# Kernel optimization log

Measured on AMD Instinct MI355X. Metric: run time of the kernel, lower is better.

The kernel has to match this reference:

```python
import jax, jax.numpy as jnp
import numpy as np

B, C, L, E = 5888, 128, 16, 10   # nodes, channels, sum(2l+1), num elements
P3, P2, P1 = 23, 4, 1            # num coupling paths per correlation order


def _sparse_u(key, shape, density=0.05):
    # U matrices are Clebsch-Gordan-derived and highly sparse
    k1, k2 = jax.random.split(key)
    vals = jax.random.normal(k1, shape, dtype=jnp.float32)
    mask = (jax.random.uniform(k2, shape) < density).astype(jnp.float32)
    return vals * mask


def setup_inputs() -> dict:
    key = jax.random.key(0)
    ks = jax.random.split(key, 8)
    x = jax.random.normal(ks[0], (B, C, L), dtype=jnp.float32)      # node features
    y = jax.random.uniform(ks[1], (B, E), dtype=jnp.float32)        # element one-hot (relaxed)
    U3 = _sparse_u(ks[2], (L, L, L, P3))
    U2 = _sparse_u(ks[3], (L, L, P2))
    U1 = _sparse_u(ks[4], (L, P1))
    w3 = jax.random.normal(ks[5], (E, P3, C), dtype=jnp.float32) / P3
    w2 = jax.random.normal(ks[6], (E, P2, C), dtype=jnp.float32) / P2
    w1 = jax.random.normal(ks[7], (E, P1, C), dtype=jnp.float32) / P1
    return {"x": x, "y": y, "U3": U3, "U2": U2, "U1": U1,
            "w3": w3, "w2": w2, "w1": w1}


def reference(x, y, U3, U2, U1, w3, w2, w1):
    # --- main contraction (nu = correlation = 3, irrep_out lmax=0) ---
    # 'wxik,ekc,bci,be->bcwx'
    out = jnp.einsum('wxik,ekc,bci,be->bcwx', U3, w3, x, y, optimize=True)  # [B,C,L,L]
    # --- nu = 2: weighting then feature contraction ---
    c = jnp.einsum('wxk,ekc,be->bcwx', U2, w2, y, optimize=True) + out      # [B,C,L,L]
    out = jnp.einsum('bcwi,bci->bcw', c, x)                                  # [B,C,L]
    # --- nu = 1 ---
    c = jnp.einsum('wk,ekc,be->bcw', U1, w1, y, optimize=True) + out        # [B,C,L]
    out = jnp.einsum('bci,bci->bc', c, x)                                    # [B,C]
    return out.reshape(out.shape[0], -1)
```

## Files before the change

kernel.cpp:

```cpp
#include <hip/hip_runtime.h>
#include <utility>

using u16 = unsigned short;
using u32 = unsigned int;

typedef float  f32x4   __attribute__((ext_vector_type(4)));
typedef float  f32x16  __attribute__((ext_vector_type(16)));
typedef __bf16 bf16x8  __attribute__((ext_vector_type(8)));

#define DI __device__ __forceinline__

struct RepT { unsigned char a, b, c, t; };
struct Tables8 {
  RepT rep[488];
  RepT slotmono[976];
  int n3, n2, n1;
};

constexpr int csort3key(int w, int x, int i) {
  int a = w, b = x, c = i, t = 0;
  if (a > b) { t = a; a = b; b = t; }
  if (b > c) { t = b; b = c; c = t; }
  if (a > b) { t = a; a = b; b = t; }
  return (a << 8) | (b << 4) | c;
}
constexpr int csort2key(int a, int b) { return a <= b ? ((a << 4) | b) : ((b << 4) | a); }

constexpr Tables8 build_tables8() {
  Tables8 T = {};
  bool used3[4096] = {};
  bool used2[256] = {};
  int nr = 0;
  for (int a = 0; a < 16; a++) for (int b = a; b < 16; b++) for (int c = b; c < 16; c++) {
    const int key  = (a << 8) | (b << 4) | c;
    const int rkey = csort3key((a + 8) & 15, (b + 8) & 15, (c + 8) & 15);
    if (rkey < key) continue;
    for (int q = 0; q < 2; q++) {
      const int kk = q ? rkey : key;
      if (!used3[kk]) {
        used3[kk] = true;
        const int f = (nr >> 3) * 16 + q * 8 + (nr & 7);
        T.slotmono[f].a = (unsigned char)(kk >> 8);
        T.slotmono[f].b = (unsigned char)((kk >> 4) & 15);
        T.slotmono[f].c = (unsigned char)(kk & 15);
        T.slotmono[f].t = 3;
      }
    }
    T.rep[nr].a = (unsigned char)a; T.rep[nr].b = (unsigned char)b;
    T.rep[nr].c = (unsigned char)c; T.rep[nr].t = 3; nr++;
  }
  T.n3 = nr;
  for (int a = 0; a < 16; a++) for (int b = a; b < 16; b++) {
    const int key  = (a << 4) | b;
    const int rkey = csort2key((a + 8) & 15, (b + 8) & 15);
    if (rkey < key) continue;
    for (int q = 0; q < 2; q++) {
      const int kk = q ? rkey : key;
      if (!used2[kk]) {
        used2[kk] = true;
        const int f = (nr >> 3) * 16 + q * 8 + (nr & 7);
        T.slotmono[f].a = (unsigned char)(kk >> 4);
        T.slotmono[f].b = (unsigned char)(kk & 15);
        T.slotmono[f].c = 0;
        T.slotmono[f].t = 2;
      }
    }
    T.rep[nr].a = (unsigned char)a; T.rep[nr].b = (unsigned char)b;
    T.rep[nr].c = 0; T.rep[nr].t = 2; nr++;
  }
  T.n2 = nr;
  for (int a = 0; a < 8; a++) {
    for (int q = 0; q < 2; q++) {
      const int f = (nr >> 3) * 16 + q * 8 + (nr & 7);
      T.slotmono[f].a = (unsigned char)((a + 8 * q) & 15);
      T.slotmono[f].b = 0; T.slotmono[f].c = 0; T.slotmono[f].t = 1;
    }
    T.rep[nr].a = (unsigned char)a; T.rep[nr].b = 0; T.rep[nr].c = 0;
    T.rep[nr].t = 1; nr++;
  }
  T.n1 = nr;
  return T;
}

constexpr Tables8 TT8 = build_tables8();
static_assert(TT8.n3 == 408, "cubic rep count");
static_assert(TT8.n2 == 480, "quad rep count");
static_assert(TT8.n1 == 488, "linear rep count");

__device__ const Tables8 g_T8 = build_tables8();

#define BN 5888
#define CN 128
#define EN 10
#define NCHUNK 61

DI u16 f2bf(float f) { union { __bf16 h; u16 s; } u; u.h = (__bf16)f; return u.s; }
DI float bf2f(u16 v) { union { u32 u; float f; } w; w.u = ((u32)v) << 16; return w.f; }

#define PREP_THREADS (NCHUNK * 64 * 8)

__global__ void prep_kernel(const float* __restrict__ U3, const float* __restrict__ U2,
                            const float* __restrict__ U1, u16* __restrict__ Sfrag16) {
  const int tid = blockIdx.x * 256 + threadIdx.x;
  if (tid >= PREP_THREADS) return;
  const int j = tid & 7, l = (tid >> 3) & 63, chunk = tid >> 9;
  const int path = l & 31, q = l >> 5;
  const RepT m = g_T8.slotmono[chunk * 16 + q * 8 + j];
  float v = 0.f;
  if (m.t == 3 && path < 23) {
    const int a = m.a, b = m.b, d = m.c;
    v = U3[((a * 16 + b) * 16 + d) * 23 + path];
    if (a == b && b == d) {
    } else if (a == b) {
      v += U3[((a * 16 + d) * 16 + a) * 23 + path]
         + U3[((d * 16 + a) * 16 + a) * 23 + path];
    } else if (b == d) {
      v += U3[((b * 16 + a) * 16 + b) * 23 + path]
         + U3[((b * 16 + b) * 16 + a) * 23 + path];
    } else {
      v += U3[((a * 16 + d) * 16 + b) * 23 + path]
         + U3[((b * 16 + a) * 16 + d) * 23 + path]
         + U3[((b * 16 + d) * 16 + a) * 23 + path]
         + U3[((d * 16 + a) * 16 + b) * 23 + path]
         + U3[((d * 16 + b) * 16 + a) * 23 + path];
    }
  } else if (m.t == 2 && path >= 23 && path < 27) {
    const int k = path - 23, a = m.a, b = m.b;
    v = U2[(a * 16 + b) * 4 + k];
    if (a != b) v += U2[(b * 16 + a) * 4 + k];
  } else if (m.t == 1 && path == 27) {
    v = U1[m.a];
  }
  Sfrag16[tid] = f2bf(v);
}

template<int R>
DI float featf(const float* xr) {
  constexpr RepT rp = TT8.rep[R];
  if constexpr (rp.t == 3) return xr[rp.a] * xr[rp.b] * xr[rp.c];
  else if constexpr (rp.t == 2) return xr[rp.a] * xr[rp.b];
  else if constexpr (rp.t == 1) return xr[rp.a];
  else return 0.f;
}

template<int C>
DI bf16x8 make_B(const float* xr) {
  bf16x8 r;
  r[0] = (__bf16)featf<C * 8 + 0>(xr);
  r[1] = (__bf16)featf<C * 8 + 1>(xr);
  r[2] = (__bf16)featf<C * 8 + 2>(xr);
  r[3] = (__bf16)featf<C * 8 + 3>(xr);
  r[4] = (__bf16)featf<C * 8 + 4>(xr);
  r[5] = (__bf16)featf<C * 8 + 5>(xr);
  r[6] = (__bf16)featf<C * 8 + 6>(xr);
  r[7] = (__bf16)featf<C * 8 + 7>(xr);
  return r;
}

template<int C>
DI void chunk_step(const uint4* sfl, const float* xr, f32x16& acc) {
  const bf16x8 B = make_B<C>(xr);
  const bf16x8 A = *reinterpret_cast<const bf16x8*>(sfl + C * 64);
  acc = __builtin_amdgcn_mfma_f32_32x32x16_bf16(A, B, acc, 0, 0, 0);
}

template<int... Cs>
DI void run_chunks(std::integer_sequence<int, Cs...>, const uint4* sfl,
                   const float* xr, f32x16& acc) {
  (chunk_step<Cs>(sfl, xr, acc), ...);
}

DI void load_xr(const float* __restrict__ x, int pair, int q, float* xr) {
  const float* base = x + pair * 16;
#pragma unroll
  for (int u = 0; u < 4; u++) {
    const int g = (u + 2 * q) & 3;
    const float4 v = *(const float4*)(base + g * 4);
    xr[u * 4 + 0] = v.x;
    xr[u * 4 + 1] = v.y;
    xr[u * 4 + 2] = v.z;
    xr[u * 4 + 3] = v.w;
  }
}

__global__ __launch_bounds__(512, 4) void main_kernel(
    const float* __restrict__ x, const float* __restrict__ y,
    const float* __restrict__ w3, const float* __restrict__ w2, const float* __restrict__ w1,
    const uint4* __restrict__ Sfrag, float* __restrict__ out)
{
  __shared__ uint4 sfrag[NCHUNK * 64];
  __shared__ u16  wbl[2][32 * 128];
  const int tid = threadIdx.x;
  const int node0 = blockIdx.x * 2;

  for (int idx = tid; idx < NCHUNK * 64; idx += 512) sfrag[idx] = Sfrag[idx];

  const int nl = tid >> 8;
  const int bnode = node0 + nl;
  {
    const int tl = tid & 255;
    const int p  = tl >> 3;
    const int c0 = (tl & 7) * 16;
    float yv[EN];
#pragma unroll
    for (int e = 0; e < EN; e++) yv[e] = y[bnode * EN + e];
    float acc[16];
#pragma unroll
    for (int m = 0; m < 16; m++) acc[m] = 0.f;
    const float* wsrc = nullptr; int stride = 0;
    if (p < 23)       { wsrc = w3 + p * 128;        stride = 23 * 128; }
    else if (p < 27)  { wsrc = w2 + (p - 23) * 128; stride = 4 * 128; }
    else if (p == 27) { wsrc = w1;                  stride = 128; }
    if (wsrc) {
      for (int e = 0; e < EN; e++) {
        const float* src = wsrc + e * stride + c0;
        const float4 v0 = *(const float4*)(src);
        const float4 v1 = *(const float4*)(src + 4);
        const float4 v2 = *(const float4*)(src + 8);
        const float4 v3 = *(const float4*)(src + 12);
        acc[0]  += yv[e] * v0.x; acc[1]  += yv[e] * v0.y;
        acc[2]  += yv[e] * v0.z; acc[3]  += yv[e] * v0.w;
        acc[4]  += yv[e] * v1.x; acc[5]  += yv[e] * v1.y;
        acc[6]  += yv[e] * v1.z; acc[7]  += yv[e] * v1.w;
        acc[8]  += yv[e] * v2.x; acc[9]  += yv[e] * v2.y;
        acc[10] += yv[e] * v2.z; acc[11] += yv[e] * v2.w;
        acc[12] += yv[e] * v3.x; acc[13] += yv[e] * v3.y;
        acc[14] += yv[e] * v3.z; acc[15] += yv[e] * v3.w;
      }
    }
#pragma unroll
    for (int m = 0; m < 16; m++) wbl[nl][p * 128 + c0 + m] = f2bf(acc[m]);
  }
  __syncthreads();

  const int w = tid >> 6, wn = w & 3;
  const int lane = tid & 63, col = lane & 31, q = lane >> 5;
  const int pair0 = bnode * 128 + wn * 32 + col;

  float xr[16];
  load_xr(x, pair0, q, xr);

  const uint4* sfl = sfrag + lane;
  f32x16 acc = {0.f, 0.f, 0.f, 0.f, 0.f, 0.f, 0.f, 0.f,
                0.f, 0.f, 0.f, 0.f, 0.f, 0.f, 0.f, 0.f};
  run_chunks(std::make_integer_sequence<int, NCHUNK>{}, sfl, xr, acc);

  const int cc = wn * 32 + col;
  float p0 = 0.f;
#pragma unroll
  for (int r = 0; r < 16; r++) {
    const int row = (r & 3) + 8 * (r >> 2) + 4 * q;
    p0 += acc[r] * bf2f(wbl[nl][row * 128 + cc]);
  }
  p0 += __shfl_xor(p0, 32);
  if (q == 0) out[pair0] = p0;
}

extern "C" void kernel_launch(void* const* d_in, const int* in_sizes, int n_in,
                              void* d_out, int out_size, void* d_ws, size_t ws_size,
                              hipStream_t stream) {
  const float* x  = (const float*)d_in[0];
  const float* y  = (const float*)d_in[1];
  const float* U3 = (const float*)d_in[2];
  const float* U2 = (const float*)d_in[3];
  const float* U1 = (const float*)d_in[4];
  const float* w3 = (const float*)d_in[5];
  const float* w2 = (const float*)d_in[6];
  const float* w1 = (const float*)d_in[7];
  u16*   Sfrag16 = (u16*)d_ws;
  float* out     = (float*)d_out;

  hipLaunchKernelGGL(prep_kernel, dim3(PREP_THREADS / 256), dim3(256), 0, stream,
                     U3, U2, U1, Sfrag16);
  hipLaunchKernelGGL(main_kernel, dim3(BN / 2), dim3(512), 0, stream,
                     x, y, w3, w2, w1, (const uint4*)d_ws, out);
}
```

Before: 179.1 us.

## Read MFMA A-fragments directly from global memory and launch one node per block

The main kernel no longer stages the precomputed sparse-U fragment table into shared memory. Each lane now loads its A fragments straight from the global workspace, relying on L1/L2 caching. Blocks shrink from 512 threads covering two nodes to 256 threads covering one node, which doubles the grid and cuts shared memory to just the per-node weight table. This removes the per-block copy and sync cost of the fragment staging and allows more resident blocks. In exchange, every MFMA step issues a global (cached) load instead of an LDS read, which may add latency.

```diff
diff --git a/kernel.cpp b/kernel.cpp
--- a/kernel.cpp
+++ b/kernel.cpp
@@ -158,16 +158,16 @@
 }
 
 template<int C>
-DI void chunk_step(const uint4* sfl, const float* xr, f32x16& acc) {
+DI void chunk_step(const uint4* __restrict__ sgl, const float* xr, f32x16& acc) {
+  const bf16x8 A = *reinterpret_cast<const bf16x8*>(sgl + C * 64);
   const bf16x8 B = make_B<C>(xr);
-  const bf16x8 A = *reinterpret_cast<const bf16x8*>(sfl + C * 64);
   acc = __builtin_amdgcn_mfma_f32_32x32x16_bf16(A, B, acc, 0, 0, 0);
 }
 
 template<int... Cs>
-DI void run_chunks(std::integer_sequence<int, Cs...>, const uint4* sfl,
+DI void run_chunks(std::integer_sequence<int, Cs...>, const uint4* __restrict__ sgl,
                    const float* xr, f32x16& acc) {
-  (chunk_step<Cs>(sfl, xr, acc), ...);
+  (chunk_step<Cs>(sgl, xr, acc), ...);
 }
 
 DI void load_xr(const float* __restrict__ x, int pair, int q, float* xr) {
@@ -183,24 +183,18 @@
   }
 }
 
-__global__ __launch_bounds__(512, 4) void main_kernel(
+__global__ __launch_bounds__(256) void main_kernel(
     const float* __restrict__ x, const float* __restrict__ y,
     const float* __restrict__ w3, const float* __restrict__ w2, const float* __restrict__ w1,
     const uint4* __restrict__ Sfrag, float* __restrict__ out)
 {
-  __shared__ uint4 sfrag[NCHUNK * 64];
-  __shared__ u16  wbl[2][32 * 128];
+  __shared__ u16 wbl[32 * 128];
   const int tid = threadIdx.x;
-  const int node0 = blockIdx.x * 2;
-
-  for (int idx = tid; idx < NCHUNK * 64; idx += 512) sfrag[idx] = Sfrag[idx];
-
-  const int nl = tid >> 8;
-  const int bnode = node0 + nl;
+  const int bnode = blockIdx.x;
+
   {
-    const int tl = tid & 255;
-    const int p  = tl >> 3;
-    const int c0 = (tl & 7) * 16;
+    const int p  = tid >> 3;
+    const int c0 = (tid & 7) * 16;
     float yv[EN];
 #pragma unroll
     for (int e = 0; e < EN; e++) yv[e] = y[bnode * EN + e];
@@ -229,28 +223,28 @@
       }
     }
 #pragma unroll
-    for (int m = 0; m < 16; m++) wbl[nl][p * 128 + c0 + m] = f2bf(acc[m]);
+    for (int m = 0; m < 16; m++) wbl[p * 128 + c0 + m] = f2bf(acc[m]);
   }
   __syncthreads();
 
-  const int w = tid >> 6, wn = w & 3;
+  const int wn = tid >> 6;
   const int lane = tid & 63, col = lane & 31, q = lane >> 5;
   const int pair0 = bnode * 128 + wn * 32 + col;
 
   float xr[16];
   load_xr(x, pair0, q, xr);
 
-  const uint4* sfl = sfrag + lane;
+  const uint4* __restrict__ sgl = Sfrag + lane;
   f32x16 acc = {0.f, 0.f, 0.f, 0.f, 0.f, 0.f, 0.f, 0.f,
                 0.f, 0.f, 0.f, 0.f, 0.f, 0.f, 0.f, 0.f};
-  run_chunks(std::make_integer_sequence<int, NCHUNK>{}, sfl, xr, acc);
+  run_chunks(std::make_integer_sequence<int, NCHUNK>{}, sgl, xr, acc);
 
   const int cc = wn * 32 + col;
   float p0 = 0.f;
 #pragma unroll
   for (int r = 0; r < 16; r++) {
     const int row = (r & 3) + 8 * (r >> 2) + 4 * q;
-    p0 += acc[r] * bf2f(wbl[nl][row * 128 + cc]);
+    p0 += acc[r] * bf2f(wbl[row * 128 + cc]);
   }
   p0 += __shfl_xor(p0, 32);
   if (q == 0) out[pair0] = p0;
@@ -272,6 +266,6 @@
 
   hipLaunchKernelGGL(prep_kernel, dim3(PREP_THREADS / 256), dim3(256), 0, stream,
                      U3, U2, U1, Sfrag16);
-  hipLaunchKernelGGL(main_kernel, dim3(BN / 2), dim3(512), 0, stream,
+  hipLaunchKernelGGL(main_kernel, dim3(BN), dim3(256), 0, stream,
                      x, y, w3, w2, w1, (const uint4*)d_ws, out);
 }
```

Result: slower. 184.5 us (+3.0%).

## Persistent grid with split LDS/global sourcing of coupling fragments

Applied to the files above, without the earlier changes.

Turns the main kernel into a persistent grid-stride loop over node pairs, so the shared coupling-fragment table is loaded once per block instead of once per pair. Only the first 36 chunks are staged in LDS; the rest are read directly from global memory (L1/L2 cached), and the two sources are interleaved in the MFMA chunk order to spread LDS and global load traffic. This cuts LDS footprint and repeated table reloads, but adds an extra barrier per iteration and depends on cache hits for the global fragments.

```diff
diff --git a/kernel.cpp b/kernel.cpp
--- a/kernel.cpp
+++ b/kernel.cpp
@@ -93,6 +93,8 @@
 #define CN 128
 #define EN 10
 #define NCHUNK 61
+#define SPLITC 36
+#define GRID 768
 
 DI u16 f2bf(float f) { union { __bf16 h; u16 s; } u; u.h = (__bf16)f; return u.s; }
 DI float bf2f(u16 v) { union { u32 u; float f; } w; w.u = ((u32)v) << 16; return w.f; }
@@ -158,16 +160,27 @@
 }
 
 template<int C>
-DI void chunk_step(const uint4* sfl, const float* xr, f32x16& acc) {
-  const bf16x8 B = make_B<C>(xr);
-  const bf16x8 A = *reinterpret_cast<const bf16x8*>(sfl + C * 64);
-  acc = __builtin_amdgcn_mfma_f32_32x32x16_bf16(A, B, acc, 0, 0, 0);
-}
-
-template<int... Cs>
-DI void run_chunks(std::integer_sequence<int, Cs...>, const uint4* sfl,
+DI void chunk_step(const uint4* sfl, const uint4* __restrict__ sgl,
                    const float* xr, f32x16& acc) {
-  (chunk_step<Cs>(sfl, xr, acc), ...);
+  if constexpr (C < SPLITC) {
+    const bf16x8 B = make_B<C>(xr);
+    const bf16x8 A = *reinterpret_cast<const bf16x8*>(sfl + C * 64);
+    acc = __builtin_amdgcn_mfma_f32_32x32x16_bf16(A, B, acc, 0, 0, 0);
+  } else {
+    const bf16x8 A = *reinterpret_cast<const bf16x8*>(sgl + C * 64);
+    const bf16x8 B = make_B<C>(xr);
+    acc = __builtin_amdgcn_mfma_f32_32x32x16_bf16(A, B, acc, 0, 0, 0);
+  }
+}
+
+constexpr int chunk_order(int i) {
+  return i < 50 ? ((i & 1) ? SPLITC + (i >> 1) : (i >> 1)) : i - 25;
+}
+
+template<int... Is>
+DI void run_chunks(std::integer_sequence<int, Is...>, const uint4* sfl,
+                   const uint4* __restrict__ sgl, const float* xr, f32x16& acc) {
+  (chunk_step<chunk_order(Is)>(sfl, sgl, xr, acc), ...);
 }
 
 DI void load_xr(const float* __restrict__ x, int pair, int q, float* xr) {
@@ -188,72 +201,80 @@
     const float* __restrict__ w3, const float* __restrict__ w2, const float* __restrict__ w1,
     const uint4* __restrict__ Sfrag, float* __restrict__ out)
 {
-  __shared__ uint4 sfrag[NCHUNK * 64];
+  __shared__ uint4 sfrag[SPLITC * 64];
   __shared__ u16  wbl[2][32 * 128];
   const int tid = threadIdx.x;
-  const int node0 = blockIdx.x * 2;
-
-  for (int idx = tid; idx < NCHUNK * 64; idx += 512) sfrag[idx] = Sfrag[idx];
+
+  for (int idx = tid; idx < SPLITC * 64; idx += 512) sfrag[idx] = Sfrag[idx];
 
   const int nl = tid >> 8;
-  const int bnode = node0 + nl;
-  {
-    const int tl = tid & 255;
-    const int p  = tl >> 3;
-    const int c0 = (tl & 7) * 16;
-    float yv[EN];
-#pragma unroll
-    for (int e = 0; e < EN; e++) yv[e] = y[bnode * EN + e];
-    float acc[16];
-#pragma unroll
-    for (int m = 0; m < 16; m++) acc[m] = 0.f;
-    const float* wsrc = nullptr; int stride = 0;
-    if (p < 23)       { wsrc = w3 + p * 128;        stride = 23 * 128; }
-    else if (p < 27)  { wsrc = w2 + (p - 23) * 128; stride = 4 * 128; }
-    else if (p == 27) { wsrc = w1;                  stride = 128; }
-    if (wsrc) {
-      for (int e = 0; e < EN; e++) {
-        const float* src = wsrc + e * stride + c0;
-        const float4 v0 = *(const float4*)(src);
-        const float4 v1 = *(const float4*)(src + 4);
-        const float4 v2 = *(const float4*)(src + 8);
-        const float4 v3 = *(const float4*)(src + 12);
-        acc[0]  += yv[e] * v0.x; acc[1]  += yv[e] * v0.y;
-        acc[2]  += yv[e] * v0.z; acc[3]  += yv[e] * v0.w;
-        acc[4]  += yv[e] * v1.x; acc[5]  += yv[e] * v1.y;
-        acc[6]  += yv[e] * v1.z; acc[7]  += yv[e] * v1.w;
-        acc[8]  += yv[e] * v2.x; acc[9]  += yv[e] * v2.y;
-        acc[10] += yv[e] * v2.z; acc[11] += yv[e] * v2.w;
-        acc[12] += yv[e] * v3.x; acc[13] += yv[e] * v3.y;
-        acc[14] += yv[e] * v3.z; acc[15] += yv[e] * v3.w;
+  const int w = tid >> 6, wn = w & 3, nw = w >> 2;
+  const int lane = tid & 63, col = lane & 31, q = lane >> 5;
+  const uint4* sfl = sfrag + lane;
+  const uint4* __restrict__ sgl = Sfrag + lane;
+
+  for (int g = blockIdx.x; g < BN / 2; g += GRID) {
+    const int node0 = g * 2;
+
+    {
+      const int bnode = node0 + nl;
+      const int tl = tid & 255;
+      const int p  = tl >> 3;
+      const int c0 = (tl & 7) * 16;
+      float yv[EN];
+#pragma unroll
+      for (int e = 0; e < EN; e++) yv[e] = y[bnode * EN + e];
+      float acc[16];
+#pragma unroll
+      for (int m = 0; m < 16; m++) acc[m] = 0.f;
+      const float* wsrc = nullptr; int stride = 0;
+      if (p < 23)       { wsrc = w3 + p * 128;        stride = 23 * 128; }
+      else if (p < 27)  { wsrc = w2 + (p - 23) * 128; stride = 4 * 128; }
+      else if (p == 27) { wsrc = w1;                  stride = 128; }
+      if (wsrc) {
+        for (int e = 0; e < EN; e++) {
+          const float* src = wsrc + e * stride + c0;
+          const float4 v0 = *(const float4*)(src);
+          const float4 v1 = *(const float4*)(src + 4);
+          const float4 v2 = *(const float4*)(src + 8);
+          const float4 v3 = *(const float4*)(src + 12);
+          acc[0]  += yv[e] * v0.x; acc[1]  += yv[e] * v0.y;
+          acc[2]  += yv[e] * v0.z; acc[3]  += yv[e] * v0.w;
+          acc[4]  += yv[e] * v1.x; acc[5]  += yv[e] * v1.y;
+          acc[6]  += yv[e] * v1.z; acc[7]  += yv[e] * v1.w;
+          acc[8]  += yv[e] * v2.x; acc[9]  += yv[e] * v2.y;
+          acc[10] += yv[e] * v2.z; acc[11] += yv[e] * v2.w;
+          acc[12] += yv[e] * v3.x; acc[13] += yv[e] * v3.y;
+          acc[14] += yv[e] * v3.z; acc[15] += yv[e] * v3.w;
+        }
       }
-    }
-#pragma unroll
-    for (int m = 0; m < 16; m++) wbl[nl][p * 128 + c0 + m] = f2bf(acc[m]);
-  }
-  __syncthreads();
-
-  const int w = tid >> 6, wn = w & 3;
-  const int lane = tid & 63, col = lane & 31, q = lane >> 5;
-  const int pair0 = bnode * 128 + wn * 32 + col;
-
-  float xr[16];
-  load_xr(x, pair0, q, xr);
-
-  const uint4* sfl = sfrag + lane;
-  f32x16 acc = {0.f, 0.f, 0.f, 0.f, 0.f, 0.f, 0.f, 0.f,
-                0.f, 0.f, 0.f, 0.f, 0.f, 0.f, 0.f, 0.f};
-  run_chunks(std::make_integer_sequence<int, NCHUNK>{}, sfl, xr, acc);
-
-  const int cc = wn * 32 + col;
-  float p0 = 0.f;
-#pragma unroll
-  for (int r = 0; r < 16; r++) {
-    const int row = (r & 3) + 8 * (r >> 2) + 4 * q;
-    p0 += acc[r] * bf2f(wbl[nl][row * 128 + cc]);
-  }
-  p0 += __shfl_xor(p0, 32);
-  if (q == 0) out[pair0] = p0;
+#pragma unroll
+      for (int m = 0; m < 16; m++) wbl[nl][p * 128 + c0 + m] = f2bf(acc[m]);
+    }
+    __syncthreads();
+
+    const int bnode = node0 + nw;
+    const int pair0 = bnode * 128 + wn * 32 + col;
+
+    float xr[16];
+    load_xr(x, pair0, q, xr);
+
+    f32x16 acc = {0.f, 0.f, 0.f, 0.f, 0.f, 0.f, 0.f, 0.f,
+                  0.f, 0.f, 0.f, 0.f, 0.f, 0.f, 0.f, 0.f};
+    run_chunks(std::make_integer_sequence<int, NCHUNK>{}, sfl, sgl, xr, acc);
+
+    const int cc = wn * 32 + col;
+    float p0 = 0.f;
+#pragma unroll
+    for (int r = 0; r < 16; r++) {
+      const int row = (r & 3) + 8 * (r >> 2) + 4 * q;
+      p0 += acc[r] * bf2f(wbl[nw][row * 128 + cc]);
+    }
+    p0 += __shfl_xor(p0, 32);
+    if (q == 0) out[pair0] = p0;
+
+    __syncthreads();
+  }
 }
 
 extern "C" void kernel_launch(void* const* d_in, const int* in_sizes, int n_in,
@@ -272,6 +293,6 @@
 
   hipLaunchKernelGGL(prep_kernel, dim3(PREP_THREADS / 256), dim3(256), 0, stream,
                      U3, U2, U1, Sfrag16);
-  hipLaunchKernelGGL(main_kernel, dim3(BN / 2), dim3(512), 0, stream,
+  hipLaunchKernelGGL(main_kernel, dim3(GRID), dim3(512), 0, stream,
                      x, y, w3, w2, w1, (const uint4*)d_ws, out);
 }
```

After: 323.1 us. +80.4%, slower.
